# Kernel optimization log

Hardware: AMD Instinct MI355X
Metric: run time of the kernel (lower is better)

Reference implementation:

```python
import jax, jax.numpy as jnp
import numpy as np

N = 10000
E = 160000
HEADS = 4
HC = 32      # hidden_channels
OC = 64      # out_channels
NG = 16      # n_goods
H1, H2 = 512, 256
NEG_SLOPE = 0.2


def setup_inputs() -> dict:
    key = jax.random.key(0)
    ks = jax.random.split(key, 32)
    rn = lambda k, s, sc=0.05: (jax.random.normal(k, s, jnp.float32) * sc)
    inp = {
        "x": jax.random.normal(ks[0], (N, 63), jnp.float32),
        "next_demand": jax.random.normal(ks[1], (N, 1), jnp.float32),
        "edge_index": jax.random.randint(ks[2], (2, E), 0, N),
        "eps": jax.random.normal(ks[3], (E, NG), jnp.float32),
        "Wl3": rn(ks[4], (HEADS * HC, 64)), "Wr3": rn(ks[5], (HEADS * HC, 64)),
        "att3": rn(ks[6], (HEADS, HC)), "b3": rn(ks[7], (HEADS * HC,)),
        # gat4: 128 -> 64, 1 head, mean
        "Wl4": rn(ks[8], (OC, HEADS * HC)), "Wr4": rn(ks[9], (OC, HEADS * HC)),
        "att4": rn(ks[10], (1, OC)), "b4": rn(ks[11], (OC,)),
        "Wl1": rn(ks[12], (HEADS * HC, OC)), "Wr1": rn(ks[13], (HEADS * HC, OC)),
        "att1": rn(ks[14], (HEADS, HC)), "b1": rn(ks[15], (HEADS * HC,)),
        # gat2: 128 -> 64, 1 head, mean
        "Wl2": rn(ks[16], (OC, HEADS * HC)), "Wr2": rn(ks[17], (OC, HEADS * HC)),
        "att2": rn(ks[18], (1, OC)), "b2": rn(ks[19], (OC,)),
        # MLP head: 256 -> 512 -> 256 -> n_goods (mu, std)
        "W_fc": rn(ks[20], (H1, OC * 4)), "b_fc": rn(ks[21], (H1,)),
        "W_fc1": rn(ks[22], (H2, H1)), "b_fc1": rn(ks[23], (H2,)),
        "W_mu": rn(ks[24], (NG, H2)), "b_mu": rn(ks[25], (NG,)),
        "W_std": rn(ks[26], (NG, H2)), "b_std": rn(ks[27], (NG,)),
    }
    return inp


def gatv2(x, src, dst, n, Wl, Wr, att, bias, heads, oc, concat):
    # GATv2Conv: e = a . LeakyReLU(Wl x_src + Wr x_dst), softmax over dst neighborhoods
    xl = (x @ Wl.T).reshape(n, heads, oc)
    xr = (x @ Wr.T).reshape(n, heads, oc)
    e = jax.nn.leaky_relu(xl[src] + xr[dst], NEG_SLOPE)        # [E', H, C]
    score = jnp.einsum('ehc,hc->eh', e, att)                   # [E', H]
    m = jax.ops.segment_max(score, dst, num_segments=n)        # stable segment softmax
    ex = jnp.exp(score - m[dst])
    den = jax.ops.segment_sum(ex, dst, num_segments=n)
    alpha = ex / (den[dst] + 1e-16)
    out = jax.ops.segment_sum(alpha[:, :, None] * xl[src], dst, num_segments=n)
    out = out.reshape(n, heads * oc) if concat else out.mean(axis=1)
    return out + bias


def reference(x, next_demand, edge_index, eps,
              Wl3, Wr3, att3, b3, Wl4, Wr4, att4, b4,
              Wl1, Wr1, att1, b1, Wl2, Wr2, att2, b2,
              W_fc, b_fc, W_fc1, b_fc1, W_mu, b_mu, W_std, b_std):
    n = x.shape[0]
    lrelu = lambda v: jax.nn.leaky_relu(v, NEG_SLOPE)
    loop = jnp.arange(n)
    # forward edges + self loops (PyG GATv2Conv add_self_loops=True)
    src = jnp.concatenate([edge_index[0], loop])
    dst = jnp.concatenate([edge_index[1], loop])
    # reverse edges + self loops
    rsrc = jnp.concatenate([edge_index[1], loop])
    rdst = jnp.concatenate([edge_index[0], loop])

    h = jnp.concatenate([x, next_demand.reshape(n, -1)], axis=1)   # [N, 64]
    xb = lrelu(gatv2(h, rsrc, rdst, n, Wl3, Wr3, att3, b3, HEADS, HC, True))
    xb = lrelu(gatv2(xb, rsrc, rdst, n, Wl4, Wr4, att4, b4, 1, OC, False))
    xf = lrelu(gatv2(xb, src, dst, n, Wl1, Wr1, att1, b1, HEADS, HC, True))
    xf = lrelu(gatv2(xf, src, dst, n, Wl2, Wr2, att2, b2, 1, OC, False))

    s = jnp.concatenate([xf, xb], axis=1)                          # [N, 128]
    se = jnp.concatenate([s[edge_index[0]], s[edge_index[1]]], axis=1)  # [E, 256]
    se = jax.nn.relu(se @ W_fc.T + b_fc)
    se = jax.nn.relu(se @ W_fc1.T + b_fc1)
    mu = se @ W_mu.T + b_mu
    std = jax.nn.softplus(se @ W_std.T + b_std)

    action = mu + std * eps                                        # rsample
    log2pi = jnp.log(2.0 * jnp.pi).astype(mu.dtype)
    lp = -0.5 * ((action - mu) / std) ** 2 - jnp.log(std) - 0.5 * log2pi
    log_prob = lp.reshape(1, -1).sum(-1, keepdims=True)            # num_graphs=1
    real_action = jnp.tanh(action)
    real_log_prob = log_prob - jnp.log(1.0 - real_action ** 2 + 1e-7).reshape(1, -1).sum(-1, keepdims=True)
    return (real_action.reshape(-1), real_log_prob)
```

## Files before the change

kernel.cpp:

```cpp
#include <hip/hip_runtime.h>
#include <hip/hip_bf16.h>
#include <math.h>

typedef __attribute__((ext_vector_type(8))) short short8;
typedef __attribute__((ext_vector_type(4))) float floatx4;

#define LRELU_S 0.2f
#define HALF_LOG_2PI 0.91893853320467274178f

__device__ __forceinline__ short f2bf(float f) {
  union { float f; unsigned u; } x; x.f = f;
  unsigned r = x.u + 0x7FFFu + ((x.u >> 16) & 1u);
  return (short)(r >> 16);
}
__device__ __forceinline__ float lrelu(float v) { return v > 0.f ? v : LRELU_S * v; }
__device__ __forceinline__ float frcp(float v) { return __builtin_amdgcn_rcpf(v); }
__device__ __forceinline__ float ftanh(float x) {
  float e = __expf(2.f * x);
  return 1.f - 2.f * frcp(e + 1.f);
}
__device__ __forceinline__ int swzb(int row) {
  return ((((row >> 2) & 3) << 1) | (row & 1)) << 4;
}

__global__ __launch_bounds__(256) void k_concat_h(const float* __restrict__ x,
    const float* __restrict__ nd, float* __restrict__ h, int total) {
  int t = blockIdx.x * 256 + threadIdx.x;
  if (t >= total) return;
  int n = t >> 6, j = t & 63;
  h[t] = (j < 63) ? x[n * 63 + j] : nd[n];
}

__global__ __launch_bounds__(256) void k_deg(const int* __restrict__ ei,
    int* __restrict__ degF, int* __restrict__ degR, int E) {
  int e = blockIdx.x * 256 + threadIdx.x;
  if (e >= E) return;
  int a = ei[e], b = ei[E + e];
  atomicAdd(degF + b, 1);
  atomicAdd(degR + a, 1);
}

__global__ __launch_bounds__(256) void k_scan2(const int* __restrict__ degF,
    int* __restrict__ startF, int* __restrict__ curF, int* __restrict__ csrF,
    const int* __restrict__ degR, int* __restrict__ startR, int* __restrict__ curR,
    int* __restrict__ csrR, int n) {
  const int* __restrict__ deg = blockIdx.x ? degR : degF;
  int* __restrict__ start = blockIdx.x ? startR : startF;
  int* __restrict__ cur   = blockIdx.x ? curR : curF;
  int* __restrict__ csr   = blockIdx.x ? csrR : csrF;
  __shared__ int part[256];
  int chunk = (n + 255) / 256;
  int t = threadIdx.x;
  int lo = t * chunk, hi = min(lo + chunk, n);
  int s = 0;
  for (int i = lo; i < hi; i++) s += deg[i] + 1;
  part[t] = s;
  __syncthreads();
  if (t == 0) {
    int acc = 0;
    for (int i = 0; i < 256; i++) { int v = part[i]; part[i] = acc; acc += v; }
    start[n] = acc;
  }
  __syncthreads();
  int acc = part[t];
  for (int i = lo; i < hi; i++) {
    start[i] = acc; cur[i] = acc;
    acc += deg[i] + 1;
    csr[acc - 1] = i;
  }
}

__global__ __launch_bounds__(256) void k_scatter(const int* __restrict__ ei,
    int* __restrict__ curF, int* __restrict__ curR,
    int* __restrict__ csrF, int* __restrict__ csrR, int E) {
  int e = blockIdx.x * 256 + threadIdx.x;
  if (e >= E) return;
  int a = ei[e], b = ei[E + e];
  int pf = atomicAdd(curF + b, 1); csrF[pf] = a;
  int pr = atomicAdd(curR + a, 1); csrR[pr] = b;
}

template<int K, int F>
__global__ __launch_bounds__(256) void k_node_gemm(const float* __restrict__ in,
    const float* __restrict__ Wl, const float* __restrict__ Wr,
    float* __restrict__ xl, float* __restrict__ xr, int n) {
  __shared__ float sx[32][K + 1];
  const int row0 = blockIdx.x * 32;
  const float* __restrict__ W = blockIdx.y ? Wr : Wl;
  float* __restrict__ out = blockIdx.y ? xr : xl;
  const int tid = threadIdx.x;
  for (int i = tid; i < 32 * K; i += 256) {
    int r = i / K, c = i - r * K;
    sx[r][c] = (row0 + r < n) ? in[(size_t)(row0 + r) * K + c] : 0.f;
  }
  __syncthreads();
  const int nl = tid & 31;
  const int fg = tid >> 5;
  const int row = row0 + nl;
  if (row >= n) return;
  constexpr int FP = F / 8;
  for (int i = 0; i < FP; i++) {
    int f = fg * FP + i;
    const float* __restrict__ wrow = W + (size_t)f * K;
    float acc = 0.f;
    #pragma unroll
    for (int k = 0; k < K; k += 4) {
      float4 wv = *(const float4*)(wrow + k);
      acc += sx[nl][k] * wv.x + sx[nl][k + 1] * wv.y
           + sx[nl][k + 2] * wv.z + sx[nl][k + 3] * wv.w;
    }
    out[(size_t)row * F + f] = acc;
  }
}

template<int HF, int C, int OM>
__global__ __launch_bounds__(256) void k_gat_fused(const float* __restrict__ XL,
    const float* __restrict__ XR, const float* __restrict__ att,
    const float* __restrict__ bias, const int* __restrict__ start,
    const int* __restrict__ csr, float* __restrict__ out,
    short* __restrict__ sout, int scol, int n) {
  constexpr int G = HF / 4;
  constexpr int DPB = 256 / G;
  int d = blockIdx.x * DPB + threadIdx.x / G;
  if (d >= n) return;
  int f4 = threadIdx.x & (G - 1);
  float4 xr = *(const float4*)(XR + (size_t)d * HF + f4 * 4);
  float4 av = *(const float4*)(att + f4 * 4);
  float4 bv = *(const float4*)(bias + f4 * 4);
  float m = -INFINITY, den = 0.f;
  float4 acc = {0.f, 0.f, 0.f, 0.f};
  int j1 = start[d + 1];
  for (int j = start[d]; j < j1; j++) {
    int s = csr[j];
    float4 xl = *(const float4*)(XL + (size_t)s * HF + f4 * 4);
    float e0 = xl.x + xr.x; e0 = e0 > 0.f ? e0 : LRELU_S * e0;
    float e1 = xl.y + xr.y; e1 = e1 > 0.f ? e1 : LRELU_S * e1;
    float e2 = xl.z + xr.z; e2 = e2 > 0.f ? e2 : LRELU_S * e2;
    float e3 = xl.w + xr.w; e3 = e3 > 0.f ? e3 : LRELU_S * e3;
    float partial = av.x * e0 + av.y * e1 + av.z * e2 + av.w * e3;
    #pragma unroll
    for (int o = C / 8; o > 0; o >>= 1) partial += __shfl_xor(partial, o, 64);
    float sc = partial;
    float mn = fmaxf(m, sc);
    float scale = __expf(m - mn);
    float p = __expf(sc - mn);
    den = den * scale + p;
    acc.x = acc.x * scale + p * xl.x;
    acc.y = acc.y * scale + p * xl.y;
    acc.z = acc.z * scale + p * xl.z;
    acc.w = acc.w * scale + p * xl.w;
    m = mn;
  }
  float inv = frcp(den + 1e-16f);
  float4 o4;
  o4.x = lrelu(acc.x * inv + bv.x);
  o4.y = lrelu(acc.y * inv + bv.y);
  o4.z = lrelu(acc.z * inv + bv.z);
  o4.w = lrelu(acc.w * inv + bv.w);
  if (OM != 2) *(float4*)(out + (size_t)d * HF + f4 * 4) = o4;
  if (OM != 0) {
    union { short s[4]; int2 v; } u;
    u.s[0] = f2bf(o4.x); u.s[1] = f2bf(o4.y);
    u.s[2] = f2bf(o4.z); u.s[3] = f2bf(o4.w);
    *(int2*)(sout + (size_t)d * 128 + scol + f4 * 4) = u.v;
  }
}

__global__ __launch_bounds__(256) void k_wconv(const float* __restrict__ Wfc,
    const float* __restrict__ Wfc1, const float* __restrict__ Wmu,
    const float* __restrict__ Wstd, short* __restrict__ WBF) {
  int t = blockIdx.x * 256 + threadIdx.x;
  if (t >= 270336) return;
  int tile = t >> 9, pos = t & 511;
  int lane = pos >> 3, j = pos & 7;
  int lr = lane & 15, lg = lane >> 4;
  float v;
  if (tile < 256) {
    int nt = tile >> 3, kk = tile & 7;
    v = Wfc[(nt * 16 + lr) * 256 + kk * 32 + lg * 8 + j];
  } else if (tile < 512) {
    int t2 = tile - 256;
    int nt = t2 >> 4, kk = t2 & 15;
    v = Wfc1[(nt * 16 + lr) * 512 + kk * 32 + lg * 8 + j];
  } else {
    int t3 = tile - 512;
    int nt = t3 >> 3, kk = t3 & 7;
    int r = nt * 16 + lr;
    int col = kk * 32 + lg * 8 + j;
    v = (r < 16) ? Wmu[r * 256 + col] : Wstd[(r - 16) * 256 + col];
  }
  WBF[t] = f2bf(v);
}

__device__ __forceinline__ short8 lds_frag(const char* base, int row, int strideB, int k0, int lg) {
  int off = row * strideB + (((k0 * 2) + lg * 16) ^ swzb(row));
  return *(const short8*)(base + off);
}

__global__ __launch_bounds__(512, 4) void k_head(
    const short* __restrict__ SBF, const short* __restrict__ WBF,
    const int* __restrict__ ei, const float* __restrict__ epsg,
    const float* __restrict__ b_fc, const float* __restrict__ b_fc1,
    const float* __restrict__ b_mu, const float* __restrict__ b_std,
    float* __restrict__ out, double* __restrict__ LP, int E) {
  __shared__ __align__(16) char lX[32768];
  __shared__ __align__(16) char cbuf[16384];
  float* lMS  = (float*)cbuf;
  float* lred = (float*)(cbuf + 8192);

  const int tid = threadIdx.x;
  const int eg0 = blockIdx.x * 64;

  for (int q = tid; q < 2048; q += 512) {
    int le = q >> 5, c = q & 31;
    int eg = eg0 + le;
    int node = (c < 16) ? ei[eg] : ei[E + eg];
    const short* srcp = SBF + (size_t)node * 128 + (c & 15) * 8;
    int4 v = *(const int4*)srcp;
    int col = (c * 16) ^ swzb(le);
    *(int4*)(lX + le * 512 + col) = v;
  }
  __syncthreads();

  const int w = tid >> 6, lane = tid & 63;
  const int lr = lane & 15, lg = lane >> 4;
  const floatx4 zero = {0.f, 0.f, 0.f, 0.f};

  floatx4 acc2[2][4];
  #pragma unroll
  for (int a = 0; a < 2; a++)
    #pragma unroll
    for (int b = 0; b < 4; b++) acc2[a][b] = zero;

  for (int c = 0; c < 4; c++) {
    floatx4 acc1[4];
    #pragma unroll
    for (int mi = 0; mi < 4; mi++) acc1[mi] = zero;
    for (int kk = 0; kk < 8; kk++) {
      int tile = (c * 8 + w) * 8 + kk;
      short8 b = *(const short8*)(WBF + tile * 512 + lane * 8);
      #pragma unroll
      for (int mi = 0; mi < 4; mi++) {
        short8 a = lds_frag(lX, mi * 16 + lr, 512, kk * 32, lg);
        acc1[mi] = __builtin_amdgcn_mfma_f32_16x16x32_bf16(a, b, acc1[mi], 0, 0, 0);
      }
    }
    __syncthreads();
    {
      int cl = w * 16 + lr;
      float bv = b_fc[c * 128 + cl];
      #pragma unroll
      for (int mi = 0; mi < 4; mi++)
        #pragma unroll
        for (int j = 0; j < 4; j++) {
          int row = mi * 16 + lg * 4 + j;
          float v = acc1[mi][j] + bv;
          v = v > 0.f ? v : 0.f;
          *(short*)(cbuf + row * 256 + ((cl * 2) ^ swzb(row))) = f2bf(v);
        }
    }
    __syncthreads();

    for (int kk2 = 0; kk2 < 4; kk2++) {
      short8 a[4];
      #pragma unroll
      for (int mi = 0; mi < 4; mi++) a[mi] = lds_frag(cbuf, mi * 16 + lr, 256, kk2 * 32, lg);
      #pragma unroll
      for (int ni2 = 0; ni2 < 2; ni2++) {
        int tile = 256 + (2 * w + ni2) * 16 + (c * 4 + kk2);
        short8 b = *(const short8*)(WBF + tile * 512 + lane * 8);
        #pragma unroll
        for (int mi = 0; mi < 4; mi++)
          acc2[ni2][mi] = __builtin_amdgcn_mfma_f32_16x16x32_bf16(a[mi], b, acc2[ni2][mi], 0, 0, 0);
      }
    }
  }
  __syncthreads();

  #pragma unroll
  for (int ni2 = 0; ni2 < 2; ni2++) {
    int n = (2 * w + ni2) * 16 + lr;
    float bv = b_fc1[n];
    #pragma unroll
    for (int mi = 0; mi < 4; mi++)
      #pragma unroll
      for (int j = 0; j < 4; j++) {
        int row = mi * 16 + lg * 4 + j;
        float v = acc2[ni2][mi][j] + bv;
        v = v > 0.f ? v : 0.f;
        *(short*)(lX + row * 512 + ((n * 2) ^ swzb(row))) = f2bf(v);
      }
  }
  __syncthreads();

  {
    const int mfr = w >> 1, nfr = w & 1;
    floatx4 acc3 = zero;
    for (int kk = 0; kk < 8; kk++) {
      short8 a = lds_frag(lX, mfr * 16 + lr, 512, kk * 32, lg);
      int tile = 512 + nfr * 8 + kk;
      short8 b = *(const short8*)(WBF + tile * 512 + lane * 8);
      acc3 = __builtin_amdgcn_mfma_f32_16x16x32_bf16(a, b, acc3, 0, 0, 0);
    }
    int coln = nfr * 16 + lr;
    float bv = (coln < 16) ? b_mu[coln] : b_std[coln - 16];
    #pragma unroll
    for (int j = 0; j < 4; j++) {
      int row = mfr * 16 + lg * 4 + j;
      lMS[row * 32 + coln] = acc3[j] + bv;
    }
  }
  __syncthreads();

  float lpsum = 0.f;
  #pragma unroll
  for (int it = 0; it < 2; it++) {
    int idx = tid + it * 512;
    int m = idx >> 4, g = idx & 15;
    float mu = lMS[m * 32 + g];
    float sr = lMS[m * 32 + 16 + g];
    float sd = (sr > 20.f) ? sr : __logf(1.f + __expf(sr));
    int eg = eg0 + m;
    float ep = epsg[(size_t)eg * 16 + g];
    float action = mu + sd * ep;
    float ra = ftanh(action);
    out[(size_t)eg * 16 + g] = ra;
    lpsum += -0.5f * ep * ep - __logf(sd) - HALF_LOG_2PI - __logf(1.f - ra * ra + 1e-7f);
  }
  #pragma unroll
  for (int o = 32; o > 0; o >>= 1) lpsum += __shfl_xor(lpsum, o, 64);
  if (lane == 0) lred[w] = lpsum;
  __syncthreads();
  if (tid == 0) {
    double ssum = 0.0;
    #pragma unroll
    for (int i = 0; i < 8; i++) ssum += (double)lred[i];
    atomicAdd(LP, ssum);
  }
}

__global__ void k_finalize(const double* __restrict__ LP, float* __restrict__ out, int pos) {
  out[pos] = (float)(*LP);
}

extern "C" void kernel_launch(void* const* d_in, const int* in_sizes, int n_in,
                              void* d_out, int out_size, void* d_ws, size_t ws_size,
                              hipStream_t stream) {
  const float* x    = (const float*)d_in[0];
  const float* nd   = (const float*)d_in[1];
  const int*   ei   = (const int*)d_in[2];
  const float* epsg = (const float*)d_in[3];
  const float* Wl3 = (const float*)d_in[4];  const float* Wr3 = (const float*)d_in[5];
  const float* att3 = (const float*)d_in[6]; const float* b3 = (const float*)d_in[7];
  const float* Wl4 = (const float*)d_in[8];  const float* Wr4 = (const float*)d_in[9];
  const float* att4 = (const float*)d_in[10]; const float* b4 = (const float*)d_in[11];
  const float* Wl1 = (const float*)d_in[12]; const float* Wr1 = (const float*)d_in[13];
  const float* att1 = (const float*)d_in[14]; const float* b1 = (const float*)d_in[15];
  const float* Wl2 = (const float*)d_in[16]; const float* Wr2 = (const float*)d_in[17];
  const float* att2 = (const float*)d_in[18]; const float* b2 = (const float*)d_in[19];
  const float* W_fc  = (const float*)d_in[20]; const float* b_fc  = (const float*)d_in[21];
  const float* W_fc1 = (const float*)d_in[22]; const float* b_fc1 = (const float*)d_in[23];
  const float* W_mu  = (const float*)d_in[24]; const float* b_mu  = (const float*)d_in[25];
  const float* W_std = (const float*)d_in[26]; const float* b_std = (const float*)d_in[27];

  const int N = in_sizes[0] / 63;
  const int E = in_sizes[2] / 2;
  const int E2 = E + N;
  const size_t NN = (size_t)N;

  char* base = (char*)d_ws;
  auto alloc = [&](size_t bytes) { char* p = base; base += (bytes + 15) & ~(size_t)15; return p; };

  float* bufA = (float*)alloc(NN * 128 * 4);
  float* bufB = (float*)alloc(NN * 128 * 4);
  float* XL   = (float*)alloc(NN * 128 * 4);
  float* XR   = (float*)alloc(NN * 128 * 4);
  float* XBp  = (float*)alloc(NN * 64 * 4);
  int* degF   = (int*)alloc(NN * 4);
  int* degR   = (int*)alloc(NN * 4);
  int* curF   = (int*)alloc(NN * 4);
  int* curR   = (int*)alloc(NN * 4);
  int* startF = (int*)alloc((NN + 1) * 4);
  int* startR = (int*)alloc((NN + 1) * 4);
  int* csrF   = (int*)alloc((size_t)E2 * 4);
  int* csrR   = (int*)alloc((size_t)E2 * 4);
  double* LPp = (double*)alloc(8);
  short* SBF  = (short*)alloc(NN * 128 * 2);
  short* WBF  = (short*)alloc(270336 * 2);

  auto nb = [](int total) { return (total + 255) / 256; };

  hipMemsetAsync(degF, 0, NN * 8, stream);
  k_deg<<<nb(E), 256, 0, stream>>>(ei, degF, degR, E);
  k_scan2<<<2, 256, 0, stream>>>(degF, startF, curF, csrF, degR, startR, curR, csrR, N);
  k_scatter<<<nb(E), 256, 0, stream>>>(ei, curF, curR, csrF, csrR, E);

  k_concat_h<<<nb(N * 64), 256, 0, stream>>>(x, nd, bufA, N * 64);
  k_wconv<<<nb(270336), 256, 0, stream>>>(W_fc, W_fc1, W_mu, W_std, WBF);

  { dim3 g((N + 31) / 32, 2);
    k_node_gemm<64, 128><<<g, 256, 0, stream>>>(bufA, Wl3, Wr3, XL, XR, N); }
  k_gat_fused<128, 32, 0><<<(N + 7) / 8, 256, 0, stream>>>(XL, XR, att3, b3, startR, csrR, bufB, nullptr, 0, N);

  { dim3 g((N + 31) / 32, 2);
    k_node_gemm<128, 64><<<g, 256, 0, stream>>>(bufB, Wl4, Wr4, XL, XR, N); }
  k_gat_fused<64, 64, 1><<<(N + 15) / 16, 256, 0, stream>>>(XL, XR, att4, b4, startR, csrR, XBp, SBF, 64, N);

  { dim3 g((N + 31) / 32, 2);
    k_node_gemm<64, 128><<<g, 256, 0, stream>>>(XBp, Wl1, Wr1, XL, XR, N); }
  k_gat_fused<128, 32, 0><<<(N + 7) / 8, 256, 0, stream>>>(XL, XR, att1, b1, startF, csrF, bufB, nullptr, 0, N);

  { dim3 g((N + 31) / 32, 2);
    k_node_gemm<128, 64><<<g, 256, 0, stream>>>(bufB, Wl2, Wr2, XL, XR, N); }
  k_gat_fused<64, 64, 2><<<(N + 15) / 16, 256, 0, stream>>>(XL, XR, att2, b2, startF, csrF, nullptr, SBF, 0, N);

  hipMemsetAsync(LPp, 0, 8, stream);
  k_head<<<E / 64, 512, 0, stream>>>(SBF, WBF, ei, epsg, b_fc, b_fc1, b_mu, b_std,
                                     (float*)d_out, LPp, E);
  k_finalize<<<1, 1, 0, stream>>>(LPp, (float*)d_out, E * 16);
}
```

Measured before the change: 479.6 us.

## Merge preprocessing kernels, parallelize scan, prefetch neighbors, fold finalize into head

Folds the degree count, input concat and weight bf16 conversion into one launch. Replaces the serial 256-entry scan with a 1024-thread wave-shuffle scan. Software-prefetches the next neighbor row in the GAT aggregation loop and unrolls the head MFMA loops. Removes the finalize kernel and the second memset by having the last head block write the log-prob through an atomic completion counter. The aim is fewer launches and less serial latency, at the cost of extra registers and a grid-completion counter protocol.

```diff
diff --git a/kernel.cpp b/kernel.cpp
--- a/kernel.cpp
+++ b/kernel.cpp
@@ -23,24 +23,54 @@
   return ((((row >> 2) & 3) << 1) | (row & 1)) << 4;
 }
 
-__global__ __launch_bounds__(256) void k_concat_h(const float* __restrict__ x,
-    const float* __restrict__ nd, float* __restrict__ h, int total) {
-  int t = blockIdx.x * 256 + threadIdx.x;
-  if (t >= total) return;
-  int n = t >> 6, j = t & 63;
-  h[t] = (j < 63) ? x[n * 63 + j] : nd[n];
-}
-
-__global__ __launch_bounds__(256) void k_deg(const int* __restrict__ ei,
-    int* __restrict__ degF, int* __restrict__ degR, int E) {
-  int e = blockIdx.x * 256 + threadIdx.x;
-  if (e >= E) return;
-  int a = ei[e], b = ei[E + e];
-  atomicAdd(degF + b, 1);
-  atomicAdd(degR + a, 1);
-}
-
-__global__ __launch_bounds__(256) void k_scan2(const int* __restrict__ degF,
+__global__ __launch_bounds__(256) void k_pre(const int* __restrict__ ei,
+    int* __restrict__ degF, int* __restrict__ degR, int E,
+    const float* __restrict__ x, const float* __restrict__ nd,
+    float* __restrict__ h, int NH,
+    const float* __restrict__ Wfc, const float* __restrict__ Wfc1,
+    const float* __restrict__ Wmu, const float* __restrict__ Wstd,
+    short* __restrict__ WBF, int nbE, int nbH) {
+  int b = blockIdx.x;
+  if (b < nbE) {
+    int e = b * 256 + threadIdx.x;
+    if (e < E) {
+      int a = ei[e], bb = ei[E + e];
+      atomicAdd(degF + bb, 1);
+      atomicAdd(degR + a, 1);
+    }
+  } else if (b < nbE + nbH) {
+    int t = (b - nbE) * 256 + threadIdx.x;
+    if (t < NH) {
+      int n = t >> 6, j = t & 63;
+      h[t] = (j < 63) ? x[n * 63 + j] : nd[n];
+    }
+  } else {
+    int t = (b - nbE - nbH) * 256 + threadIdx.x;
+    if (t < 270336) {
+      int tile = t >> 9, pos = t & 511;
+      int lane = pos >> 3, j = pos & 7;
+      int lr = lane & 15, lg = lane >> 4;
+      float v;
+      if (tile < 256) {
+        int nt = tile >> 3, kk = tile & 7;
+        v = Wfc[(nt * 16 + lr) * 256 + kk * 32 + lg * 8 + j];
+      } else if (tile < 512) {
+        int t2 = tile - 256;
+        int nt = t2 >> 4, kk = t2 & 15;
+        v = Wfc1[(nt * 16 + lr) * 512 + kk * 32 + lg * 8 + j];
+      } else {
+        int t3 = tile - 512;
+        int nt = t3 >> 3, kk = t3 & 7;
+        int r = nt * 16 + lr;
+        int col = kk * 32 + lg * 8 + j;
+        v = (r < 16) ? Wmu[r * 256 + col] : Wstd[(r - 16) * 256 + col];
+      }
+      WBF[t] = f2bf(v);
+    }
+  }
+}
+
+__global__ __launch_bounds__(1024) void k_scan2(const int* __restrict__ degF,
     int* __restrict__ startF, int* __restrict__ curF, int* __restrict__ csrF,
     const int* __restrict__ degR, int* __restrict__ startR, int* __restrict__ curR,
     int* __restrict__ csrR, int n) {
@@ -48,21 +78,35 @@
   int* __restrict__ start = blockIdx.x ? startR : startF;
   int* __restrict__ cur   = blockIdx.x ? curR : curF;
   int* __restrict__ csr   = blockIdx.x ? csrR : csrF;
-  __shared__ int part[256];
-  int chunk = (n + 255) / 256;
+  __shared__ int wsum[16];
   int t = threadIdx.x;
-  int lo = t * chunk, hi = min(lo + chunk, n);
+  int chunk = (n + 1023) >> 10;
+  int lo = t * chunk; if (lo > n) lo = n;
+  int hi = lo + chunk; if (hi > n) hi = n;
   int s = 0;
   for (int i = lo; i < hi; i++) s += deg[i] + 1;
-  part[t] = s;
-  __syncthreads();
-  if (t == 0) {
-    int acc = 0;
-    for (int i = 0; i < 256; i++) { int v = part[i]; part[i] = acc; acc += v; }
-    start[n] = acc;
-  }
-  __syncthreads();
-  int acc = part[t];
+  int lane = t & 63, wv = t >> 6;
+  int inc = s;
+  #pragma unroll
+  for (int o = 1; o < 64; o <<= 1) {
+    int v = __shfl_up(inc, o, 64);
+    if (lane >= o) inc += v;
+  }
+  if (lane == 63) wsum[wv] = inc;
+  __syncthreads();
+  if (t < 64) {
+    int v = (t < 16) ? wsum[t] : 0;
+    #pragma unroll
+    for (int o = 1; o < 16; o <<= 1) {
+      int u = __shfl_up(v, o, 64);
+      if (t >= o) v += u;
+    }
+    if (t < 16) wsum[t] = v;
+  }
+  __syncthreads();
+  int base = (wv ? wsum[wv - 1] : 0) + (inc - s);
+  if (t == 0) start[n] = wsum[15];
+  int acc = base;
   for (int i = lo; i < hi; i++) {
     start[i] = acc; cur[i] = acc;
     acc += deg[i] + 1;
@@ -129,10 +173,15 @@
   float4 bv = *(const float4*)(bias + f4 * 4);
   float m = -INFINITY, den = 0.f;
   float4 acc = {0.f, 0.f, 0.f, 0.f};
-  int j1 = start[d + 1];
-  for (int j = start[d]; j < j1; j++) {
-    int s = csr[j];
-    float4 xl = *(const float4*)(XL + (size_t)s * HF + f4 * 4);
+  int j0 = start[d], j1 = start[d + 1];
+  int s0 = csr[j0];
+  float4 xl = *(const float4*)(XL + (size_t)s0 * HF + f4 * 4);
+  for (int j = j0; j < j1; j++) {
+    float4 xln = xl;
+    if (j + 1 < j1) {
+      int sn = csr[j + 1];
+      xln = *(const float4*)(XL + (size_t)sn * HF + f4 * 4);
+    }
     float e0 = xl.x + xr.x; e0 = e0 > 0.f ? e0 : LRELU_S * e0;
     float e1 = xl.y + xr.y; e1 = e1 > 0.f ? e1 : LRELU_S * e1;
     float e2 = xl.z + xr.z; e2 = e2 > 0.f ? e2 : LRELU_S * e2;
@@ -150,6 +199,7 @@
     acc.z = acc.z * scale + p * xl.z;
     acc.w = acc.w * scale + p * xl.w;
     m = mn;
+    xl = xln;
   }
   float inv = frcp(den + 1e-16f);
   float4 o4;
@@ -166,32 +216,6 @@
   }
 }
 
-__global__ __launch_bounds__(256) void k_wconv(const float* __restrict__ Wfc,
-    const float* __restrict__ Wfc1, const float* __restrict__ Wmu,
-    const float* __restrict__ Wstd, short* __restrict__ WBF) {
-  int t = blockIdx.x * 256 + threadIdx.x;
-  if (t >= 270336) return;
-  int tile = t >> 9, pos = t & 511;
-  int lane = pos >> 3, j = pos & 7;
-  int lr = lane & 15, lg = lane >> 4;
-  float v;
-  if (tile < 256) {
-    int nt = tile >> 3, kk = tile & 7;
-    v = Wfc[(nt * 16 + lr) * 256 + kk * 32 + lg * 8 + j];
-  } else if (tile < 512) {
-    int t2 = tile - 256;
-    int nt = t2 >> 4, kk = t2 & 15;
-    v = Wfc1[(nt * 16 + lr) * 512 + kk * 32 + lg * 8 + j];
-  } else {
-    int t3 = tile - 512;
-    int nt = t3 >> 3, kk = t3 & 7;
-    int r = nt * 16 + lr;
-    int col = kk * 32 + lg * 8 + j;
-    v = (r < 16) ? Wmu[r * 256 + col] : Wstd[(r - 16) * 256 + col];
-  }
-  WBF[t] = f2bf(v);
-}
-
 __device__ __forceinline__ short8 lds_frag(const char* base, int row, int strideB, int k0, int lg) {
   int off = row * strideB + (((k0 * 2) + lg * 16) ^ swzb(row));
   return *(const short8*)(base + off);
@@ -202,7 +226,8 @@
     const int* __restrict__ ei, const float* __restrict__ epsg,
     const float* __restrict__ b_fc, const float* __restrict__ b_fc1,
     const float* __restrict__ b_mu, const float* __restrict__ b_std,
-    float* __restrict__ out, double* __restrict__ LP, int E) {
+    float* __restrict__ out, double* __restrict__ LP, unsigned* __restrict__ CTR,
+    int E) {
   __shared__ __align__(16) char lX[32768];
   __shared__ __align__(16) char cbuf[16384];
   float* lMS  = (float*)cbuf;
@@ -236,6 +261,7 @@
     floatx4 acc1[4];
     #pragma unroll
     for (int mi = 0; mi < 4; mi++) acc1[mi] = zero;
+    #pragma unroll
     for (int kk = 0; kk < 8; kk++) {
       int tile = (c * 8 + w) * 8 + kk;
       short8 b = *(const short8*)(WBF + tile * 512 + lane * 8);
@@ -261,6 +287,7 @@
     }
     __syncthreads();
 
+    #pragma unroll
     for (int kk2 = 0; kk2 < 4; kk2++) {
       short8 a[4];
       #pragma unroll
@@ -296,6 +323,7 @@
   {
     const int mfr = w >> 1, nfr = w & 1;
     floatx4 acc3 = zero;
+    #pragma unroll
     for (int kk = 0; kk < 8; kk++) {
       short8 a = lds_frag(lX, mfr * 16 + lr, 512, kk * 32, lg);
       int tile = 512 + nfr * 8 + kk;
@@ -336,11 +364,14 @@
     #pragma unroll
     for (int i = 0; i < 8; i++) ssum += (double)lred[i];
     atomicAdd(LP, ssum);
-  }
-}
-
-__global__ void k_finalize(const double* __restrict__ LP, float* __restrict__ out, int pos) {
-  out[pos] = (float)(*LP);
+    __threadfence();
+    unsigned old = atomicAdd(CTR, 1u);
+    if (old == gridDim.x - 1) {
+      __threadfence();
+      double v = *(volatile double*)LP;
+      out[(size_t)E * 16] = (float)v;
+    }
+  }
 }
 
 extern "C" void kernel_launch(void* const* d_in, const int* in_sizes, int n_in,
@@ -371,32 +402,33 @@
   char* base = (char*)d_ws;
   auto alloc = [&](size_t bytes) { char* p = base; base += (bytes + 15) & ~(size_t)15; return p; };
 
+  int* degF   = (int*)alloc(NN * 4);
+  int* degR   = (int*)alloc(NN * 4);
+  double* LPp = (double*)alloc(16);
+  unsigned* CTRp = (unsigned*)(LPp + 1);
   float* bufA = (float*)alloc(NN * 128 * 4);
   float* bufB = (float*)alloc(NN * 128 * 4);
   float* XL   = (float*)alloc(NN * 128 * 4);
   float* XR   = (float*)alloc(NN * 128 * 4);
   float* XBp  = (float*)alloc(NN * 64 * 4);
-  int* degF   = (int*)alloc(NN * 4);
-  int* degR   = (int*)alloc(NN * 4);
   int* curF   = (int*)alloc(NN * 4);
   int* curR   = (int*)alloc(NN * 4);
   int* startF = (int*)alloc((NN + 1) * 4);
   int* startR = (int*)alloc((NN + 1) * 4);
   int* csrF   = (int*)alloc((size_t)E2 * 4);
   int* csrR   = (int*)alloc((size_t)E2 * 4);
-  double* LPp = (double*)alloc(8);
   short* SBF  = (short*)alloc(NN * 128 * 2);
   short* WBF  = (short*)alloc(270336 * 2);
 
   auto nb = [](int total) { return (total + 255) / 256; };
-
-  hipMemsetAsync(degF, 0, NN * 8, stream);
-  k_deg<<<nb(E), 256, 0, stream>>>(ei, degF, degR, E);
-  k_scan2<<<2, 256, 0, stream>>>(degF, startF, curF, csrF, degR, startR, curR, csrR, N);
-  k_scatter<<<nb(E), 256, 0, stream>>>(ei, curF, curR, csrF, csrR, E);
-
-  k_concat_h<<<nb(N * 64), 256, 0, stream>>>(x, nd, bufA, N * 64);
-  k_wconv<<<nb(270336), 256, 0, stream>>>(W_fc, W_fc1, W_mu, W_std, WBF);
+  const int nbE = nb(E), nbH = nb(N * 64), nbW = nb(270336);
+
+  hipMemsetAsync(degF, 0, NN * 8 + 16, stream);
+
+  k_pre<<<nbE + nbH + nbW, 256, 0, stream>>>(ei, degF, degR, E, x, nd, bufA, N * 64,
+                                             W_fc, W_fc1, W_mu, W_std, WBF, nbE, nbH);
+  k_scan2<<<2, 1024, 0, stream>>>(degF, startF, curF, csrF, degR, startR, curR, csrR, N);
+  k_scatter<<<nbE, 256, 0, stream>>>(ei, curF, curR, csrF, csrR, E);
 
   { dim3 g((N + 31) / 32, 2);
     k_node_gemm<64, 128><<<g, 256, 0, stream>>>(bufA, Wl3, Wr3, XL, XR, N); }
@@ -414,8 +446,6 @@
     k_node_gemm<128, 64><<<g, 256, 0, stream>>>(bufB, Wl2, Wr2, XL, XR, N); }
   k_gat_fused<64, 64, 2><<<(N + 15) / 16, 256, 0, stream>>>(XL, XR, att2, b2, startF, csrF, nullptr, SBF, 0, N);
 
-  hipMemsetAsync(LPp, 0, 8, stream);
   k_head<<<E / 64, 512, 0, stream>>>(SBF, WBF, ei, epsg, b_fc, b_fc1, b_mu, b_std,
-                                     (float*)d_out, LPp, E);
-  k_finalize<<<1, 1, 0, stream>>>(LPp, (float*)d_out, E * 16);
-}
+                                     (float*)d_out, LPp, CTRp, E);
+}
```

Result: slower. 513.2 us (+7.0%).
